# Kernel tuning notes

Hardware: AMD Instinct MI355X
Metric: run time of the kernel (lower is better)

Reference implementation:

```python
import jax, jax.numpy as jnp
import numpy as np

DIM = 768
B, N = 16, 1024
EPS_LN = 1e-5

def _layernorm(x, gamma, beta):
    mu = jnp.mean(x, axis=-1, keepdims=True)
    var = jnp.mean((x - mu) ** 2, axis=-1, keepdims=True)
    return (x - mu) * jax.lax.rsqrt(var + EPS_LN) * gamma + beta

def _gelu(x):
    return jax.nn.gelu(x, approximate=False)

def setup_inputs() -> dict:
    key = jax.random.key(0)
    ks = jax.random.split(key, 10)
    d = DIM
    s1 = 1.0 / np.sqrt(2 * d)
    s = 1.0 / np.sqrt(d)
    return {
        "x": jax.random.normal(ks[0], (B, N, d), dtype=jnp.float32),
        "gamma": jnp.ones((d,), jnp.float32),
        "beta": jnp.zeros((d,), jnp.float32),
        "w1": jax.random.normal(ks[1], (2 * d, d), jnp.float32) * s1,
        "b1": jnp.zeros((d,), jnp.float32),
        "w2": jax.random.normal(ks[2], (d, d), jnp.float32) * s,
        "b2": jnp.zeros((d,), jnp.float32),
        "w3": jax.random.normal(ks[3], (d, d), jnp.float32) * s,
        "b3": jnp.zeros((d,), jnp.float32),
        "w4": jax.random.normal(ks[4], (d, d), jnp.float32) * s,
        "b4": jnp.zeros((d,), jnp.float32),
    }

def reference(x, gamma, beta, w1, b1, w2, b2, w3, b3, w4, b4):
    # x: [B, N, D]
    avg_x = jnp.mean(x, axis=1)                      # [B, D]
    A = avg_x[:, None, :] * jax.nn.sigmoid(_layernorm(x, gamma, beta))  # [B, N, D]
    # batched pairwise Euclidean distance among tokens (replaces python loop)
    sq = jnp.sum(A * A, axis=-1)                     # [B, N]
    d2 = sq[:, :, None] + sq[:, None, :] - 2.0 * jnp.einsum('bnd,bmd->bnm', A, A)
    dist = jnp.sqrt(jnp.clip(d2, 1e-12))             # [B, N, N]
    m = jnp.max(dist, axis=-1)                       # [B, N]
    m_x = x + m[..., None]                           # [B, N, D]
    cat = jnp.concatenate([A, m_x], axis=-1)         # [B, N, 2D]
    m1 = _gelu(cat @ w1 + b1)                        # layer1
    W = _gelu(m1 @ w2 + b2)                          # layer2
    Wdyn = x * W
    l3 = _gelu((m1 * Wdyn) @ w3 + b3)                # layer3
    out = _gelu((x * l3) @ w4 + b4)                  # layer4
    return out.astype(jnp.float32)
```

## Files before the change

### kernel.cpp

```cpp
#include <hip/hip_runtime.h>
#include <hip/hip_fp16.h>
#include <math.h>

#define DIM 768
#define NTOK 1024
#define NBATCH 16
#define BNR (NBATCH * NTOK)

typedef _Float16 f16x8 __attribute__((ext_vector_type(8)));
typedef float f32x4 __attribute__((ext_vector_type(4)));

__device__ __forceinline__ void gl2lds16(const void* g, void* l) {
    __builtin_amdgcn_global_load_lds(
        (const __attribute__((address_space(1))) void*)g,
        (__attribute__((address_space(3))) void*)l, 16, 0, 0);
}

__device__ __forceinline__ float gelu_fast(float z) {
    const float s = z * 0.70710678118654752f;
    const float ax = fabsf(s);
    const float t = __builtin_amdgcn_rcpf(1.0f + 0.3275911f * ax);
    const float poly = t * (0.254829592f + t * (-0.284496736f +
                       t * (1.421413741f + t * (-1.453152027f + t * 1.061405429f))));
    const float e = __expf(-ax * ax);
    float erfv = 1.0f - poly * e;
    erfv = copysignf(erfv, s);
    return 0.5f * z * (1.0f + erfv);
}

__global__ __launch_bounds__(256) void avg_kernel(const float* __restrict__ x,
                                                  float* __restrict__ avgx) {
    const int d = blockIdx.x * 256 + threadIdx.x;
    const int b = blockIdx.y;
    const int n0 = blockIdx.z * 128;
    const float* xp = x + (size_t)b * NTOK * DIM + (size_t)n0 * DIM + d;
    float s = 0.0f;
    for (int n = 0; n < 128; ++n) s += xp[(size_t)n * DIM];
    atomicAdd(&avgx[b * DIM + d], s * (1.0f / NTOK));
}

__global__ __launch_bounds__(256) void colsum_w1b(const float* __restrict__ w1,
                                                  float* __restrict__ s1) {
    const int col = blockIdx.x * 256 + threadIdx.x;
    const int r0 = 768 + blockIdx.y * 64;
    float s = 0.0f;
    #pragma unroll 8
    for (int r = 0; r < 64; ++r) s += w1[(size_t)(r0 + r) * 768 + col];
    atomicAdd(&s1[col], s);
}

__global__ __launch_bounds__(256) void ln_sig_kernel(
    const float* __restrict__ x, const float* __restrict__ gamma,
    const float* __restrict__ beta, const float* __restrict__ avgx,
    __half* __restrict__ Ah, __half* __restrict__ xh, float* __restrict__ sq)
{
    const int wv = threadIdx.x >> 6, lane = threadIdx.x & 63;
    const int row = blockIdx.x * 4 + wv;
    const int b = row >> 10;
    const float* xr = x + (size_t)row * DIM;
    float4 v[3];
    #pragma unroll
    for (int i = 0; i < 3; ++i) v[i] = *(const float4*)&xr[i * 256 + lane * 4];
    float s = v[0].x + v[0].y + v[0].z + v[0].w
            + v[1].x + v[1].y + v[1].z + v[1].w
            + v[2].x + v[2].y + v[2].z + v[2].w;
    #pragma unroll
    for (int o = 32; o > 0; o >>= 1) s += __shfl_xor(s, o, 64);
    const float mu = s * (1.0f / DIM);
    float ss = 0.0f;
    #pragma unroll
    for (int i = 0; i < 3; ++i) {
        const float dx0 = v[i].x - mu, dx1 = v[i].y - mu, dx2 = v[i].z - mu, dx3 = v[i].w - mu;
        ss += dx0 * dx0 + dx1 * dx1 + dx2 * dx2 + dx3 * dx3;
    }
    #pragma unroll
    for (int o = 32; o > 0; o >>= 1) ss += __shfl_xor(ss, o, 64);
    const float rstd = rsqrtf(ss * (1.0f / DIM) + 1e-5f);
    float qs = 0.0f;
    #pragma unroll
    for (int i = 0; i < 3; ++i) {
        const int d0 = i * 256 + lane * 4;
        const float4 g4 = *(const float4*)&gamma[d0];
        const float4 b4 = *(const float4*)&beta[d0];
        const float4 a4 = *(const float4*)&avgx[b * DIM + d0];
        ushort4 pa, px;
        const float xv[4] = {v[i].x, v[i].y, v[i].z, v[i].w};
        const float gv[4] = {g4.x, g4.y, g4.z, g4.w};
        const float bv[4] = {b4.x, b4.y, b4.z, b4.w};
        const float av[4] = {a4.x, a4.y, a4.z, a4.w};
        unsigned short pav[4], pxv[4];
        #pragma unroll
        for (int j = 0; j < 4; ++j) {
            const float ln = (xv[j] - mu) * rstd * gv[j] + bv[j];
            const float sg = 1.0f / (1.0f + expf(-ln));
            const float a = av[j] * sg;
            const __half h = __float2half(a);
            const float ar = __half2float(h);
            qs += ar * ar;
            pav[j] = __half_as_ushort(h);
            pxv[j] = __half_as_ushort(__float2half(xv[j]));
        }
        pa.x = pav[0]; pa.y = pav[1]; pa.z = pav[2]; pa.w = pav[3];
        px.x = pxv[0]; px.y = pxv[1]; px.z = pxv[2]; px.w = pxv[3];
        *(ushort4*)&Ah[(size_t)row * DIM + d0] = pa;
        *(ushort4*)&xh[(size_t)row * DIM + d0] = px;
    }
    #pragma unroll
    for (int o = 32; o > 0; o >>= 1) qs += __shfl_xor(qs, o, 64);
    if (lane == 0) sq[row] = qs;
}

__device__ __forceinline__ void wconv_body(const float* __restrict__ w,
                                           __half* __restrict__ wT, int K, int N,
                                           int bx, int by)
{
    __shared__ float t[64][65];
    const int k0 = by * 64, n0 = bx * 64;
    const int tid = threadIdx.x;
    const int r = tid >> 4, c4 = (tid & 15) * 4;
    #pragma unroll
    for (int p = 0; p < 4; ++p) {
        const int rr = p * 16 + r;
        const float4 v = *(const float4*)&w[(size_t)(k0 + rr) * N + n0 + c4];
        t[rr][c4] = v.x; t[rr][c4 + 1] = v.y; t[rr][c4 + 2] = v.z; t[rr][c4 + 3] = v.w;
    }
    __syncthreads();
    #pragma unroll
    for (int p = 0; p < 4; ++p) {
        const int nn = p * 16 + r;
        ushort4 pk;
        pk.x = __half_as_ushort(__float2half(t[c4 + 0][nn]));
        pk.y = __half_as_ushort(__float2half(t[c4 + 1][nn]));
        pk.z = __half_as_ushort(__float2half(t[c4 + 2][nn]));
        pk.w = __half_as_ushort(__float2half(t[c4 + 3][nn]));
        *(ushort4*)&wT[(size_t)(n0 + nn) * K + k0 + c4] = pk;
    }
}

__global__ __launch_bounds__(256) void wconv(const float* __restrict__ w,
                                             __half* __restrict__ wT, int K, int N)
{
    wconv_body(w, wT, K, N, blockIdx.x, blockIdx.y);
}

__global__ __launch_bounds__(256) void wconv3(const float* __restrict__ w2,
                                              const float* __restrict__ w3,
                                              const float* __restrict__ w4,
                                              __half* __restrict__ t2,
                                              __half* __restrict__ t3,
                                              __half* __restrict__ t4)
{
    const float* w = (blockIdx.z == 0) ? w2 : (blockIdx.z == 1) ? w3 : w4;
    __half* wT = (blockIdx.z == 0) ? t2 : (blockIdx.z == 1) ? t3 : t4;
    wconv_body(w, wT, 768, 768, blockIdx.x, blockIdx.y);
}

template<int K, bool CAT, int EPI>
__global__ __launch_bounds__(256, 4) void gemm16(
    const __half* __restrict__ A0, const __half* __restrict__ A1,
    const __half* __restrict__ BT, const float* __restrict__ bias,
    const float* __restrict__ xin, const __half* __restrict__ m1h,
    const float* __restrict__ mv, const float* __restrict__ sv,
    __half* __restrict__ outH, float* __restrict__ outF)
{
    __shared__ _Float16 As[2][128 * 32];
    __shared__ _Float16 Bs[2][128 * 32];
    const int tid = threadIdx.x;
    const int w = tid >> 6, lane = tid & 63;
    const int wu = __builtin_amdgcn_readfirstlane(w);
    const int wr = w >> 1, wc = w & 1;
    const int R0 = blockIdx.x * 128, J0 = blockIdx.y * 128;
    constexpr int rs = CAT ? DIM : K;
    const int srow = lane >> 2;
    const int sk8 = (((lane & 3) ^ ((lane >> 3) & 3))) * 8;
    const int fx = ((lane >> 4) ^ ((lane >> 1) & 3)) * 8;
    constexpr int NT = K / 32;

    f32x4 acc[4][4];
    #pragma unroll
    for (int mt = 0; mt < 4; ++mt)
        #pragma unroll
        for (int nt = 0; nt < 4; ++nt) {
            f32x4 z = {0.0f, 0.0f, 0.0f, 0.0f};
            acc[mt][nt] = z;
        }

    auto stage = [&](int buf, int k0) {
        const __half* Ab = (CAT && k0 >= DIM) ? (A1 + (k0 - DIM)) : (A0 + k0);
        #pragma unroll
        for (int i = 0; i < 2; ++i) {
            const int rbase = i * 64 + w * 16;
            const int rbu = i * 64 + wu * 16;
            gl2lds16(Ab + (size_t)(R0 + rbase + srow) * rs + sk8, &As[buf][rbu * 32]);
            gl2lds16(BT + (size_t)(J0 + rbase + srow) * K + k0 + sk8, &Bs[buf][rbu * 32]);
        }
    };

    stage(0, 0);
    __syncthreads();
    #pragma unroll 2
    for (int kt = 0; kt < NT; ++kt) {
        const int cur = kt & 1;
        if (kt + 1 < NT) stage(cur ^ 1, (kt + 1) * 32);
        f16x8 af[4], bf[4];
        #pragma unroll
        for (int mt = 0; mt < 4; ++mt)
            af[mt] = *(const f16x8*)&As[cur][(wr * 64 + mt * 16 + (lane & 15)) * 32 + fx];
        #pragma unroll
        for (int nt = 0; nt < 4; ++nt)
            bf[nt] = *(const f16x8*)&Bs[cur][(wc * 64 + nt * 16 + (lane & 15)) * 32 + fx];
        #pragma unroll
        for (int mt = 0; mt < 4; ++mt)
            #pragma unroll
            for (int nt = 0; nt < 4; ++nt)
                acc[mt][nt] = __builtin_amdgcn_mfma_f32_16x16x32_f16(af[mt], bf[nt], acc[mt][nt], 0, 0, 0);
        __syncthreads();
    }

    #pragma unroll
    for (int mt = 0; mt < 4; ++mt) {
        float mrow[4];
        if constexpr (EPI == 0) {
            #pragma unroll
            for (int r = 0; r < 4; ++r)
                mrow[r] = mv[R0 + wr * 64 + mt * 16 + (lane >> 4) * 4 + r];
        }
        #pragma unroll
        for (int nt = 0; nt < 4; ++nt) {
            const int col = J0 + wc * 64 + nt * 16 + (lane & 15);
            const float bv = bias[col];
            float s1c = 0.0f;
            if constexpr (EPI == 0) s1c = sv[col];
            #pragma unroll
            for (int r = 0; r < 4; ++r) {
                const int row = R0 + wr * 64 + mt * 16 + (lane >> 4) * 4 + r;
                const size_t off = (size_t)row * DIM + col;
                if (EPI == 0) {
                    const float g = gelu_fast(acc[mt][nt][r] + bv + mrow[r] * s1c);
                    outH[off] = __float2half(g);
                } else if (EPI == 1) {
                    const float g = gelu_fast(acc[mt][nt][r] + bv);
                    outH[off] = __float2half(__half2float(m1h[off]) * xin[off] * g);
                } else if (EPI == 2) {
                    const float g = gelu_fast(acc[mt][nt][r] + bv);
                    outH[off] = __float2half(xin[off] * g);
                } else {
                    outF[off] = gelu_fast(acc[mt][nt][r] + bv);
                }
            }
        }
    }
}

__global__ __launch_bounds__(256, 4) void dist16(const __half* __restrict__ Ah,
                                                 const float* __restrict__ sq,
                                                 float* __restrict__ m)
{
    __shared__ _Float16 As[2][128 * 32];
    __shared__ _Float16 Bs[2][128 * 32];
    const int tid = threadIdx.x;
    const int w = tid >> 6, lane = tid & 63;
    const int wu = __builtin_amdgcn_readfirstlane(w);
    const int wr = w >> 1, wc = w & 1;
    const int base = blockIdx.x * NTOK;
    int t = blockIdx.y, ty = 0;
    while (t >= 8 - ty) { t -= 8 - ty; ++ty; }
    const int tz = ty + t;
    const int I0 = ty * 128, J0 = tz * 128;
    const int srow = lane >> 2;
    const int sk8 = (((lane & 3) ^ ((lane >> 3) & 3))) * 8;
    const int fx = ((lane >> 4) ^ ((lane >> 1) & 3)) * 8;
    constexpr int NT = DIM / 32;

    f32x4 acc[4][4];
    #pragma unroll
    for (int mt = 0; mt < 4; ++mt)
        #pragma unroll
        for (int nt = 0; nt < 4; ++nt) {
            f32x4 z = {0.0f, 0.0f, 0.0f, 0.0f};
            acc[mt][nt] = z;
        }

    auto stage = [&](int buf, int k0) {
        #pragma unroll
        for (int i = 0; i < 2; ++i) {
            const int rbase = i * 64 + w * 16;
            const int rbu = i * 64 + wu * 16;
            gl2lds16(Ah + (size_t)(base + I0 + rbase + srow) * DIM + k0 + sk8, &As[buf][rbu * 32]);
            gl2lds16(Ah + (size_t)(base + J0 + rbase + srow) * DIM + k0 + sk8, &Bs[buf][rbu * 32]);
        }
    };

    stage(0, 0);
    __syncthreads();
    #pragma unroll 2
    for (int kt = 0; kt < NT; ++kt) {
        const int cur = kt & 1;
        if (kt + 1 < NT) stage(cur ^ 1, (kt + 1) * 32);
        f16x8 af[4], bf[4];
        #pragma unroll
        for (int mt = 0; mt < 4; ++mt)
            af[mt] = *(const f16x8*)&As[cur][(wr * 64 + mt * 16 + (lane & 15)) * 32 + fx];
        #pragma unroll
        for (int nt = 0; nt < 4; ++nt)
            bf[nt] = *(const f16x8*)&Bs[cur][(wc * 64 + nt * 16 + (lane & 15)) * 32 + fx];
        #pragma unroll
        for (int mt = 0; mt < 4; ++mt)
            #pragma unroll
            for (int nt = 0; nt < 4; ++nt)
                acc[mt][nt] = __builtin_amdgcn_mfma_f32_16x16x32_f16(af[mt], bf[nt], acc[mt][nt], 0, 0, 0);
        __syncthreads();
    }

    float sqiA[4][4];
    #pragma unroll
    for (int mt = 0; mt < 4; ++mt)
        #pragma unroll
        for (int r = 0; r < 4; ++r)
            sqiA[mt][r] = sq[base + I0 + wr * 64 + mt * 16 + (lane >> 4) * 4 + r];
    float sqjA[4];
    #pragma unroll
    for (int nt = 0; nt < 4; ++nt)
        sqjA[nt] = sq[base + J0 + wc * 64 + nt * 16 + (lane & 15)];

    #pragma unroll
    for (int mt = 0; mt < 4; ++mt) {
        float vmax[4] = {-1e30f, -1e30f, -1e30f, -1e30f};
        #pragma unroll
        for (int nt = 0; nt < 4; ++nt)
            #pragma unroll
            for (int r = 0; r < 4; ++r)
                vmax[r] = fmaxf(vmax[r], sqiA[mt][r] + sqjA[nt] - 2.0f * acc[mt][nt][r]);
        #pragma unroll
        for (int r = 0; r < 4; ++r) {
            float v = vmax[r];
            v = fmaxf(v, __shfl_xor(v, 1, 64));
            v = fmaxf(v, __shfl_xor(v, 2, 64));
            v = fmaxf(v, __shfl_xor(v, 4, 64));
            v = fmaxf(v, __shfl_xor(v, 8, 64));
            if ((lane & 15) == 0) {
                const float d = sqrtf(fmaxf(v, 1e-12f));
                atomicMax((unsigned int*)&m[base + I0 + wr * 64 + mt * 16 + (lane >> 4) * 4 + r],
                          __float_as_uint(d));
            }
        }
    }

    if (I0 != J0) {
        #pragma unroll
        for (int nt = 0; nt < 4; ++nt) {
            float cm = -1e30f;
            #pragma unroll
            for (int mt = 0; mt < 4; ++mt)
                #pragma unroll
                for (int r = 0; r < 4; ++r)
                    cm = fmaxf(cm, sqiA[mt][r] + sqjA[nt] - 2.0f * acc[mt][nt][r]);
            cm = fmaxf(cm, __shfl_xor(cm, 16, 64));
            cm = fmaxf(cm, __shfl_xor(cm, 32, 64));
            if ((lane >> 4) == 0) {
                const float d = sqrtf(fmaxf(cm, 1e-12f));
                atomicMax((unsigned int*)&m[base + J0 + wc * 64 + nt * 16 + (lane & 15)],
                          __float_as_uint(d));
            }
        }
    }
}

extern "C" void kernel_launch(void* const* d_in, const int* in_sizes, int n_in,
                              void* d_out, int out_size, void* d_ws, size_t ws_size,
                              hipStream_t stream)
{
    const float* x     = (const float*)d_in[0];
    const float* gamma = (const float*)d_in[1];
    const float* beta  = (const float*)d_in[2];
    const float* w1    = (const float*)d_in[3];
    const float* b1    = (const float*)d_in[4];
    const float* w2    = (const float*)d_in[5];
    const float* b2    = (const float*)d_in[6];
    const float* w3    = (const float*)d_in[7];
    const float* b3    = (const float*)d_in[8];
    const float* w4    = (const float*)d_in[9];
    const float* b4    = (const float*)d_in[10];
    float* out = (float*)d_out;
    float* ws  = (float*)d_ws;

    float* avgx = ws;
    float* mbuf = ws + 12288;
    float* s1   = mbuf + 16384;
    float* sq   = s1 + 768;
    __half* w1T = (__half*)(sq + 16384);
    __half* w2T = w1T + (size_t)1536 * 768;
    __half* w3T = w2T + (size_t)768 * 768;
    __half* w4T = w3T + (size_t)768 * 768;
    __half* P0  = w4T + (size_t)768 * 768;
    __half* P1  = P0 + (size_t)BNR * DIM;
    __half* Ah  = (__half*)d_out;
    __half* xh  = Ah + (size_t)BNR * DIM;

    hipMemsetAsync(ws, 0, (12288 + 16384 + 768) * sizeof(float), stream);
    wconv<<<dim3(12, 24), 256, 0, stream>>>(w1, w1T, 1536, 768);
    wconv3<<<dim3(12, 12, 3), 256, 0, stream>>>(w2, w3, w4, w2T, w3T, w4T);
    colsum_w1b<<<dim3(3, 12), 256, 0, stream>>>(w1, s1);
    avg_kernel<<<dim3(3, NBATCH, 8), 256, 0, stream>>>(x, avgx);
    ln_sig_kernel<<<BNR / 4, 256, 0, stream>>>(x, gamma, beta, avgx, Ah, xh, sq);
    dist16<<<dim3(NBATCH, 36), 256, 0, stream>>>(Ah, sq, mbuf);
    gemm16<1536, true, 0><<<dim3(128, 6), 256, 0, stream>>>(
        Ah, xh, w1T, b1, nullptr, nullptr, mbuf, s1, P0, nullptr);
    gemm16<768, false, 1><<<dim3(128, 6), 256, 0, stream>>>(
        P0, nullptr, w2T, b2, x, P0, nullptr, nullptr, P1, nullptr);
    gemm16<768, false, 2><<<dim3(128, 6), 256, 0, stream>>>(
        P1, nullptr, w3T, b3, x, nullptr, nullptr, nullptr, P0, nullptr);
    gemm16<768, false, 3><<<dim3(128, 6), 256, 0, stream>>>(
        P0, nullptr, w4T, b4, x, nullptr, nullptr, nullptr, nullptr, out);
}
```

Baseline: 328.7 us.

## Enlarge GEMM tiles to 256x192 with 512 threads and BK=64

Replaces the 128x128 GEMM tile (256 threads, BK=32) with a 256x192 tile using 8 waves and a K-step of 64, with a new XOR swizzle for the wider LDS rows. Each wave now computes a 64x96 sub-tile (4x6 MFMA fragments), which raises arithmetic intensity per LDS and global load and halves the number of k-iterations and barriers. The cost is more LDS per block (about 112 KB double-buffered), more accumulator registers, and only 256 blocks per GEMM, which may underfill the 256 CUs and limit latency hiding.

```diff
diff --git a/kernel.cpp b/kernel.cpp
--- a/kernel.cpp
+++ b/kernel.cpp
@@ -156,31 +156,30 @@
 }
 
 template<int K, bool CAT, int EPI>
-__global__ __launch_bounds__(256, 4) void gemm16(
+__global__ __launch_bounds__(512, 2) void gemm256(
     const __half* __restrict__ A0, const __half* __restrict__ A1,
     const __half* __restrict__ BT, const float* __restrict__ bias,
     const float* __restrict__ xin, const __half* __restrict__ m1h,
     const float* __restrict__ mv, const float* __restrict__ sv,
     __half* __restrict__ outH, float* __restrict__ outF)
 {
-    __shared__ _Float16 As[2][128 * 32];
-    __shared__ _Float16 Bs[2][128 * 32];
+    __shared__ _Float16 As[2][256 * 64];
+    __shared__ _Float16 Bs[2][192 * 64];
     const int tid = threadIdx.x;
     const int w = tid >> 6, lane = tid & 63;
     const int wu = __builtin_amdgcn_readfirstlane(w);
     const int wr = w >> 1, wc = w & 1;
-    const int R0 = blockIdx.x * 128, J0 = blockIdx.y * 128;
+    const int R0 = blockIdx.x * 256, J0 = blockIdx.y * 192;
     constexpr int rs = CAT ? DIM : K;
-    const int srow = lane >> 2;
-    const int sk8 = (((lane & 3) ^ ((lane >> 3) & 3))) * 8;
-    const int fx = ((lane >> 4) ^ ((lane >> 1) & 3)) * 8;
-    constexpr int NT = K / 32;
-
-    f32x4 acc[4][4];
+    const int srow = lane >> 3;
+    const int soct = ((lane & 7) ^ ((lane >> 3) & 7)) * 8;
+    constexpr int NT = K / 64;
+
+    f32x4 acc[4][6];
     #pragma unroll
     for (int mt = 0; mt < 4; ++mt)
         #pragma unroll
-        for (int nt = 0; nt < 4; ++nt) {
+        for (int nt = 0; nt < 6; ++nt) {
             f32x4 z = {0.0f, 0.0f, 0.0f, 0.0f};
             acc[mt][nt] = z;
         }
@@ -188,11 +187,16 @@
     auto stage = [&](int buf, int k0) {
         const __half* Ab = (CAT && k0 >= DIM) ? (A1 + (k0 - DIM)) : (A0 + k0);
         #pragma unroll
-        for (int i = 0; i < 2; ++i) {
-            const int rbase = i * 64 + w * 16;
-            const int rbu = i * 64 + wu * 16;
-            gl2lds16(Ab + (size_t)(R0 + rbase + srow) * rs + sk8, &As[buf][rbu * 32]);
-            gl2lds16(BT + (size_t)(J0 + rbase + srow) * K + k0 + sk8, &Bs[buf][rbu * 32]);
+        for (int o = 0; o < 4; ++o) {
+            const int r = o * 64 + w * 8 + srow;
+            const int ru = o * 64 + wu * 8;
+            gl2lds16(Ab + (size_t)(R0 + r) * rs + soct, &As[buf][ru * 64]);
+        }
+        #pragma unroll
+        for (int o = 0; o < 3; ++o) {
+            const int r = o * 64 + w * 8 + srow;
+            const int ru = o * 64 + wu * 8;
+            gl2lds16(BT + (size_t)(J0 + r) * K + k0 + soct, &Bs[buf][ru * 64]);
         }
     };
 
@@ -201,19 +205,28 @@
     #pragma unroll 2
     for (int kt = 0; kt < NT; ++kt) {
         const int cur = kt & 1;
-        if (kt + 1 < NT) stage(cur ^ 1, (kt + 1) * 32);
-        f16x8 af[4], bf[4];
-        #pragma unroll
-        for (int mt = 0; mt < 4; ++mt)
-            af[mt] = *(const f16x8*)&As[cur][(wr * 64 + mt * 16 + (lane & 15)) * 32 + fx];
-        #pragma unroll
-        for (int nt = 0; nt < 4; ++nt)
-            bf[nt] = *(const f16x8*)&Bs[cur][(wc * 64 + nt * 16 + (lane & 15)) * 32 + fx];
-        #pragma unroll
-        for (int mt = 0; mt < 4; ++mt)
-            #pragma unroll
-            for (int nt = 0; nt < 4; ++nt)
-                acc[mt][nt] = __builtin_amdgcn_mfma_f32_16x16x32_f16(af[mt], bf[nt], acc[mt][nt], 0, 0, 0);
+        if (kt + 1 < NT) stage(cur ^ 1, (kt + 1) * 64);
+        #pragma unroll
+        for (int kh = 0; kh < 2; ++kh) {
+            f16x8 af[4], bf[6];
+            #pragma unroll
+            for (int mt = 0; mt < 4; ++mt) {
+                const int row = wr * 64 + mt * 16 + (lane & 15);
+                const int oct = (kh * 4 + (lane >> 4)) ^ (row & 7);
+                af[mt] = *(const f16x8*)&As[cur][row * 64 + oct * 8];
+            }
+            #pragma unroll
+            for (int nt = 0; nt < 6; ++nt) {
+                const int row = wc * 96 + nt * 16 + (lane & 15);
+                const int oct = (kh * 4 + (lane >> 4)) ^ (row & 7);
+                bf[nt] = *(const f16x8*)&Bs[cur][row * 64 + oct * 8];
+            }
+            #pragma unroll
+            for (int mt = 0; mt < 4; ++mt)
+                #pragma unroll
+                for (int nt = 0; nt < 6; ++nt)
+                    acc[mt][nt] = __builtin_amdgcn_mfma_f32_16x16x32_f16(af[mt], bf[nt], acc[mt][nt], 0, 0, 0);
+        }
         __syncthreads();
     }
 
@@ -226,8 +239,8 @@
                 mrow[r] = mv[R0 + wr * 64 + mt * 16 + (lane >> 4) * 4 + r];
         }
         #pragma unroll
-        for (int nt = 0; nt < 4; ++nt) {
-            const int col = J0 + wc * 64 + nt * 16 + (lane & 15);
+        for (int nt = 0; nt < 6; ++nt) {
+            const int col = J0 + wc * 96 + nt * 16 + (lane & 15);
             const float bv = bias[col];
             float s1c = 0.0f;
             if constexpr (EPI == 0) s1c = sv[col];
@@ -404,12 +417,12 @@
     avg_kernel<<<dim3(3, NBATCH, 8), 256, 0, stream>>>(x, avgx);
     ln_sig_kernel<<<BNR / 4, 256, 0, stream>>>(x, gamma, beta, avgx, Ah, xh, sq);
     dist16<<<dim3(NBATCH, 36), 256, 0, stream>>>(Ah, sq, mbuf);
-    gemm16<1536, true, 0><<<dim3(128, 6), 256, 0, stream>>>(
+    gemm256<1536, true, 0><<<dim3(64, 4), 512, 0, stream>>>(
         Ah, xh, w1T, b1, nullptr, nullptr, mbuf, s1, P0, nullptr);
-    gemm16<768, false, 1><<<dim3(128, 6), 256, 0, stream>>>(
+    gemm256<768, false, 1><<<dim3(64, 4), 512, 0, stream>>>(
         P0, nullptr, w2T, b2, x, P0, nullptr, nullptr, P1, nullptr);
-    gemm16<768, false, 2><<<dim3(128, 6), 256, 0, stream>>>(
+    gemm256<768, false, 2><<<dim3(64, 4), 512, 0, stream>>>(
         P1, nullptr, w3T, b3, x, nullptr, nullptr, nullptr, P0, nullptr);
-    gemm16<768, false, 3><<<dim3(128, 6), 256, 0, stream>>>(
+    gemm256<768, false, 3><<<dim3(64, 4), 512, 0, stream>>>(
         P0, nullptr, w4T, b4, x, nullptr, nullptr, nullptr, nullptr, out);
 }
```

After: 326.2 us. Within noise of the previous version (-0.8%).
